# Kernel optimization log

Hardware: AMD Instinct MI355X
Metric: run time of the kernel (lower is better)

## Reference

```python
import jax, jax.numpy as jnp
import numpy as np
import math

V, D, H, F, L, S, B = 50257, 1024, 16, 4096, 4, 2048, 2
DK = D // H

def setup_inputs() -> dict:
    key = jax.random.key(0)
    ks = iter(jax.random.split(key, 32))
    std = 0.02
    def nrm(shape):
        return (std * jax.random.normal(next(ks), shape)).astype(jnp.float32)
    inp = {
        "x": jax.random.randint(next(ks), (B, S), 0, V, dtype=jnp.int32),
        "emb": nrm((V, D)),
        "ln1_g": jnp.ones((L, D), jnp.float32), "ln1_b": jnp.zeros((L, D), jnp.float32),
        "wq": nrm((L, D, D)), "wk": nrm((L, D, D)), "wv": nrm((L, D, D)), "wo": nrm((L, D, D)),
        "ln2_g": jnp.ones((L, D), jnp.float32), "ln2_b": jnp.zeros((L, D), jnp.float32),
        "w1": nrm((L, D, F)), "b1": jnp.zeros((L, F), jnp.float32),
        "w2": nrm((L, F, D)), "b2": jnp.zeros((L, D), jnp.float32),
        "lnf_g": jnp.ones((D,), jnp.float32), "lnf_b": jnp.zeros((D,), jnp.float32),
        "head_w": nrm((D, V)), "head_b": jnp.zeros((V,), jnp.float32),
    }
    return inp

def _layernorm(x, g, b, eps=1e-5):
    mu = jnp.mean(x, axis=-1, keepdims=True)
    var = jnp.var(x, axis=-1, keepdims=True)
    return (x - mu) * jax.lax.rsqrt(var + eps) * g + b

def _posenc(seq_len, d_model, dtype):
    pos = jnp.arange(seq_len, dtype=jnp.float32)[:, None]                  # [S,1]
    div = jnp.exp(jnp.arange(0, d_model, 2, dtype=jnp.float32) * (-math.log(10000.0) / d_model))
    ang = pos * div                                                        # [S,D/2]
    pe = jnp.stack([jnp.sin(ang), jnp.cos(ang)], axis=-1).reshape(seq_len, d_model)
    return pe.astype(dtype)

def reference(x, emb, ln1_g, ln1_b, wq, wk, wv, wo, ln2_g, ln2_b, w1, b1, w2, b2, lnf_g, lnf_b, head_w, head_b):
    b, s = x.shape
    h = emb[x] + _posenc(s, D, emb.dtype)[None]                            # [B,S,D]
    causal = jnp.tril(jnp.ones((s, s), dtype=bool))                       # True = keep
    scale = 1.0 / math.sqrt(DK)
    neg_inf = jnp.finfo(h.dtype).min
    for l in range(L):
        # --- attention sublayer ---
        hn = _layernorm(h, ln1_g[l], ln1_b[l])
        q = (hn @ wq[l]).reshape(b, s, H, DK)
        k = (hn @ wk[l]).reshape(b, s, H, DK)
        v = (hn @ wv[l]).reshape(b, s, H, DK)
        scores = jnp.einsum("bqhd,bkhd->bhqk", q, k) * scale
        scores = jnp.where(causal[None, None], scores, neg_inf)
        w = jax.nn.softmax(scores, axis=-1)
        attn = jnp.einsum("bhqk,bkhd->bqhd", w, v).reshape(b, s, D)
        h = h + attn @ wo[l]
        # --- FFN sublayer ---
        hn = _layernorm(h, ln2_g[l], ln2_b[l])
        h = h + jax.nn.relu(hn @ w1[l] + b1[l]) @ w2[l] + b2[l]
    h = _layernorm(h, lnf_g, lnf_b)
    logits = h @ head_w + head_b                                           # [B,S,V]
    return logits
```

## Files before the change

### kernel.cpp

```cpp
#include <hip/hip_runtime.h>
#include <math.h>

#define VOCAB 50257
#define VPAD  50432
#define DM    1024
#define NH    16
#define DKH   64
#define FF    4096
#define NL    4
#define SEQ   2048
#define BATCH 2
#define MROWS (BATCH*SEQ)

typedef __bf16 bf16_t;
typedef __bf16 bf16x8 __attribute__((ext_vector_type(8)));
typedef __bf16 bf16x4 __attribute__((ext_vector_type(4)));
typedef float  f32x4  __attribute__((ext_vector_type(4)));

typedef void as1_void __attribute__((address_space(1)));
typedef void as3_void __attribute__((address_space(3)));

__device__ __forceinline__ void gload_lds16(const void* g, void* l) {
  __builtin_amdgcn_global_load_lds((as1_void*)g, (as3_void*)l, 16, 0, 0);
}

__device__ __forceinline__ uint32_t lds_addr32(const void* p) {
  return (uint32_t)(uintptr_t)(as3_void*)p;
}

__device__ __forceinline__ bf16x8 dsr128(uint32_t addr) {
  bf16x8 v;
  asm volatile("ds_read_b128 %0, %1" : "=v"(v) : "v"(addr));
  return v;
}

#define FENCE asm volatile("" ::: "memory")
#define BAR() do { FENCE; __builtin_amdgcn_s_barrier(); FENCE; } while (0)
#define LGKM0_FENCE() do { \
  asm volatile("s_waitcnt lgkmcnt(0)" ::: "memory"); \
  __builtin_amdgcn_sched_barrier(0); \
} while (0)

__global__ __launch_bounds__(256) void embed_kernel(const int* __restrict__ x,
    const float* __restrict__ emb, float* __restrict__ h) {
  int row = blockIdx.x;
  int s = row & (SEQ - 1);
  int d = threadIdx.x * 4;
  const float* e = emb + (size_t)x[row] * DM + d;
  float4 v = *(const float4*)e;
  float vin[4] = {v.x, v.y, v.z, v.w};
  float out[4];
#pragma unroll
  for (int j = 0; j < 4; ++j) {
    int dd = d + j;
    int i = dd >> 1;
    float freq = expf(-0.017988946039016376f * (float)i);
    float ang = (float)s * freq;
    float pe = (dd & 1) ? cosf(ang) : sinf(ang);
    out[j] = vin[j] + pe;
  }
  *(float4*)(h + (size_t)row * DM + d) = make_float4(out[0], out[1], out[2], out[3]);
}

__global__ __launch_bounds__(256) void ln_kernel(const float* __restrict__ x,
    const float* __restrict__ g, const float* __restrict__ b, bf16_t* __restrict__ out) {
  int row = blockIdx.x;
  int tid = threadIdx.x, lane = tid & 63, wave = tid >> 6;
  const float* xr = x + (size_t)row * DM;
  float4 v = ((const float4*)xr)[tid];
  float s1 = v.x + v.y + v.z + v.w;
  float s2 = v.x * v.x + v.y * v.y + v.z * v.z + v.w * v.w;
#pragma unroll
  for (int d = 1; d < 64; d <<= 1) { s1 += __shfl_xor(s1, d); s2 += __shfl_xor(s2, d); }
  __shared__ float red[8];
  if (lane == 0) { red[wave] = s1; red[4 + wave] = s2; }
  __syncthreads();
  s1 = red[0] + red[1] + red[2] + red[3];
  s2 = red[4] + red[5] + red[6] + red[7];
  float mu = s1 * (1.0f / DM);
  float var = s2 * (1.0f / DM) - mu * mu;
  float rs = rsqrtf(var + 1e-5f);
  float4 gv = ((const float4*)g)[tid];
  float4 bv = ((const float4*)b)[tid];
  bf16x4 o;
  o[0] = (bf16_t)((v.x - mu) * rs * gv.x + bv.x);
  o[1] = (bf16_t)((v.y - mu) * rs * gv.y + bv.y);
  o[2] = (bf16_t)((v.z - mu) * rs * gv.z + bv.z);
  o[3] = (bf16_t)((v.w - mu) * rs * gv.w + bv.w);
  *(bf16x4*)(out + (size_t)row * DM + tid * 4) = o;
}

__global__ __launch_bounds__(256) void transpose_cast_kernel(const float* __restrict__ in,
    bf16_t* __restrict__ out, int K, int N, int Npad) {
  __shared__ float tile[32][33];
  int n0 = blockIdx.x * 32, k0 = blockIdx.y * 32;
  int tx = threadIdx.x & 31, ty = threadIdx.x >> 5;
#pragma unroll
  for (int kk = ty; kk < 32; kk += 8) {
    int n = n0 + tx;
    tile[kk][tx] = (n < N) ? in[(size_t)(k0 + kk) * N + n] : 0.f;
  }
  __syncthreads();
#pragma unroll
  for (int nn = ty; nn < 32; nn += 8) {
    out[(size_t)(n0 + nn) * K + k0 + tx] = (bf16_t)tile[tx][nn];
  }
}

__global__ __launch_bounds__(256) void vtrans_kernel(const bf16_t* __restrict__ qkv,
    bf16_t* __restrict__ vT) {
  int sb = blockIdx.x, hh = blockIdx.y, bb = blockIdx.z;
  __shared__ bf16_t t[64][72];
  int tid = threadIdx.x;
  const bf16_t* src = qkv + ((size_t)bb * SEQ + sb * 64) * (3 * DM) + 2 * DM + hh * DKH;
#pragma unroll
  for (int c = 0; c < 2; ++c) {
    int u = c * 256 + tid;
    int s = u >> 3, d8 = u & 7;
    *(bf16x8*)&t[s][d8 * 8] = *(const bf16x8*)(src + (size_t)s * (3 * DM) + d8 * 8);
  }
  __syncthreads();
  bf16_t* dst = vT + ((size_t)(bb * NH + hh) * DKH) * SEQ + sb * 64;
#pragma unroll
  for (int c = 0; c < 2; ++c) {
    int u = c * 256 + tid;
    int dk = u >> 3, s8 = u & 7;
    bf16x8 v;
#pragma unroll
    for (int j = 0; j < 8; ++j) v[j] = t[s8 * 8 + j][dk];
    *(bf16x8*)(dst + (size_t)dk * SEQ + s8 * 8) = v;
  }
}

__global__ __launch_bounds__(256) void gemm_kernel(
    const bf16_t* __restrict__ A, const bf16_t* __restrict__ Bt, int K,
    const float* __restrict__ bias, const float* __restrict__ Rsd,
    float* Cf, bf16_t* Cb, int ldc, int Nvalid, int relu) {
  __shared__ __align__(16) bf16_t lA[4096];
  __shared__ __align__(16) bf16_t lB[4096];
  int tid = threadIdx.x, lane = tid & 63, wave = tid >> 6;
  int g = lane >> 4, r = lane & 15;
  int wr = wave >> 1, wc = wave & 1;
  int m0 = blockIdx.x * 128, n0 = blockIdx.y * 128;

  f32x4 zero = {0.f, 0.f, 0.f, 0.f};
  f32x4 acc[4][4];
#pragma unroll
  for (int i = 0; i < 4; ++i)
#pragma unroll
    for (int j = 0; j < 4; ++j) acc[i][j] = zero;

  const bf16_t* Abase = A + (size_t)m0 * K;
  const bf16_t* Bbase = Bt + (size_t)n0 * K;

  for (int k0 = 0; k0 < K; k0 += 32) {
    __syncthreads();
#pragma unroll
    for (int c = 0; c < 2; ++c) {
      int u = c * 256 + tid;
      int k8 = u >> 7, rw = u & 127;
      gload_lds16(Abase + (size_t)rw * K + k0 + k8 * 8, &lA[(c * 256 + wave * 64) * 8]);
      gload_lds16(Bbase + (size_t)rw * K + k0 + k8 * 8, &lB[(c * 256 + wave * 64) * 8]);
    }
    __syncthreads();
    bf16x8 af[4], bfr[4];
#pragma unroll
    for (int mr = 0; mr < 4; ++mr)
      af[mr] = *(const bf16x8*)&lA[(g * 128 + wr * 64 + mr * 16 + r) * 8];
#pragma unroll
    for (int nr = 0; nr < 4; ++nr)
      bfr[nr] = *(const bf16x8*)&lB[(g * 128 + wc * 64 + nr * 16 + r) * 8];
#pragma unroll
    for (int mr = 0; mr < 4; ++mr)
#pragma unroll
      for (int nr = 0; nr < 4; ++nr)
        acc[mr][nr] = __builtin_amdgcn_mfma_f32_16x16x32_bf16(af[mr], bfr[nr], acc[mr][nr], 0, 0, 0);
  }

#pragma unroll
  for (int mr = 0; mr < 4; ++mr) {
    int row = m0 + wr * 64 + mr * 16 + g * 4;
#pragma unroll
    for (int nr = 0; nr < 4; ++nr) {
      int col = n0 + wc * 64 + nr * 16 + r;
      if (col < Nvalid) {
        float bval = bias ? bias[col] : 0.f;
#pragma unroll
        for (int i = 0; i < 4; ++i) {
          float vv = acc[mr][nr][i] + bval;
          if (relu) vv = fmaxf(vv, 0.f);
          size_t idx = (size_t)(row + i) * ldc + col;
          if (Rsd) vv += Rsd[idx];
          if (Cf) Cf[idx] = vv;
          if (Cb) Cb[idx] = (bf16_t)vv;
        }
      }
    }
  }
}

__global__ __launch_bounds__(512, 2) void gemm256_kernel(
    const bf16_t* __restrict__ A, const bf16_t* __restrict__ Bt, int K,
    const float* __restrict__ bias, float* Cf, bf16_t* Cb,
    int ldc, int Nvalid, int relu, int gridM, int gridN) {
  __shared__ __align__(16) bf16_t lds[65536];

  int nwg = gridM * gridN;
  int orig = blockIdx.x;
  int q = nwg >> 3, rr = nwg & 7;
  int xcd = orig & 7, idx = orig >> 3;
  int swz = (xcd < rr ? xcd * (q + 1) : rr * (q + 1) + (xcd - rr) * q) + idx;
  int bm = swz % gridM, bn = swz / gridM;
  int m0 = bm * 256, n0 = bn * 256;

  int tid = threadIdx.x, lane = tid & 63, wave = tid >> 6;
  int g = lane >> 4, r = lane & 15;
  int wr = wave >> 2, wc = wave & 3;

  f32x4 zero = {0.f, 0.f, 0.f, 0.f};
  f32x4 acc[8][4];
#pragma unroll
  for (int i = 0; i < 8; ++i)
#pragma unroll
    for (int j = 0; j < 4; ++j) acc[i][j] = zero;

  const bf16_t* Ab = A + (size_t)m0 * K;
  const bf16_t* Bb = Bt + (size_t)n0 * K;
  int NT = K >> 6;

  uint32_t L0 = lds_addr32(lds);
  uint32_t laneOff = (uint32_t)(g * 2048 + r * 16);
  uint32_t aBase0 = L0 + ((uint32_t)wr << 14) + laneOff;
  uint32_t bBase0 = L0 + 65536u + ((uint32_t)(wc >> 1) << 14) + laneOff
                  + (uint32_t)((wc & 1) * 1024);

  auto stageA = [&](int t, int hh) {
    int b = t & 1, k0 = t << 6;
    const bf16_t* src = Ab + (size_t)(hh * 128) * K + k0;
    bf16_t* dst = lds + (size_t)(b * 2 + hh) * 8192;
#pragma unroll
    for (int j = 0; j < 2; ++j) {
      int u = j * 512 + tid;
      gload_lds16(src + (size_t)(u & 127) * K + (u >> 7) * 8, dst + (j * 512 + wave * 64) * 8);
    }
  };
  auto stageB = [&](int t, int hh) {
    int b = t & 1, k0 = t << 6;
    const bf16_t* src = Bb + (size_t)(hh * 128) * K + k0;
    bf16_t* dst = lds + 32768 + (size_t)(b * 2 + hh) * 8192;
#pragma unroll
    for (int j = 0; j < 2; ++j) {
      int u = j * 512 + tid;
      gload_lds16(src + (size_t)(u & 127) * K + (u >> 7) * 8, dst + (j * 512 + wave * 64) * 8);
    }
  };

  stageB(0, 0); stageB(0, 1); stageA(0, 0); stageA(0, 1);
  if (NT > 1) {
    stageB(1, 0); stageB(1, 1);
    asm volatile("s_waitcnt vmcnt(4)" ::: "memory");
  } else {
    asm volatile("s_waitcnt vmcnt(0)" ::: "memory");
  }
  BAR();

  for (int t = 0; t < NT; ++t) {
    uint32_t bsel = (uint32_t)((t & 1) << 15);
    uint32_t Aaddr = aBase0 + bsel;
    uint32_t Baddr = bBase0 + bsel;

    bf16x8 a0[4][2], a1[4][2], b01[2][2], b23[2][2];

#pragma unroll
    for (int mi = 0; mi < 4; ++mi)
#pragma unroll
      for (int kk = 0; kk < 2; ++kk)
        a0[mi][kk] = dsr128(Aaddr + (uint32_t)(kk * 8192 + mi * 256));
#pragma unroll
    for (int ni = 0; ni < 2; ++ni)
#pragma unroll
      for (int kk = 0; kk < 2; ++kk)
        b01[ni][kk] = dsr128(Baddr + (uint32_t)(kk * 8192 + ni * 256));
    if (t + 1 < NT) stageA(t + 1, 0);
    BAR();
    LGKM0_FENCE();
    __builtin_amdgcn_s_setprio(1);
#pragma unroll
    for (int mi = 0; mi < 4; ++mi)
#pragma unroll
      for (int ni = 0; ni < 2; ++ni)
#pragma unroll
        for (int kk = 0; kk < 2; ++kk)
          acc[mi][ni] = __builtin_amdgcn_mfma_f32_16x16x32_bf16(a0[mi][kk], b01[ni][kk], acc[mi][ni], 0, 0, 0);
    __builtin_amdgcn_s_setprio(0);
    __builtin_amdgcn_sched_barrier(0);
    BAR();

#pragma unroll
    for (int ni = 0; ni < 2; ++ni)
#pragma unroll
      for (int kk = 0; kk < 2; ++kk)
        b23[ni][kk] = dsr128(Baddr + (uint32_t)(kk * 8192 + (ni + 2) * 256));
    if (t + 1 < NT) stageA(t + 1, 1);
    BAR();
    LGKM0_FENCE();
    __builtin_amdgcn_s_setprio(1);
#pragma unroll
    for (int mi = 0; mi < 4; ++mi)
#pragma unroll
      for (int ni = 0; ni < 2; ++ni)
#pragma unroll
        for (int kk = 0; kk < 2; ++kk)
          acc[mi][ni + 2] = __builtin_amdgcn_mfma_f32_16x16x32_bf16(a0[mi][kk], b23[ni][kk], acc[mi][ni + 2], 0, 0, 0);
    __builtin_amdgcn_s_setprio(0);
    __builtin_amdgcn_sched_barrier(0);
    BAR();

#pragma unroll
    for (int mi = 0; mi < 4; ++mi)
#pragma unroll
      for (int kk = 0; kk < 2; ++kk)
        a1[mi][kk] = dsr128(Aaddr + (uint32_t)(kk * 8192 + (mi + 4) * 256));
    if (t + 2 < NT) stageB(t + 2, 0);
    BAR();
    LGKM0_FENCE();
    __builtin_amdgcn_s_setprio(1);
#pragma unroll
    for (int mi = 0; mi < 4; ++mi)
#pragma unroll
      for (int ni = 0; ni < 2; ++ni)
#pragma unroll
        for (int kk = 0; kk < 2; ++kk)
          acc[mi + 4][ni] = __builtin_amdgcn_mfma_f32_16x16x32_bf16(a1[mi][kk], b01[ni][kk], acc[mi + 4][ni], 0, 0, 0);
    __builtin_amdgcn_s_setprio(0);
    __builtin_amdgcn_sched_barrier(0);
    BAR();

    if (t + 2 < NT) stageB(t + 2, 1);
    __builtin_amdgcn_sched_barrier(0);
    __builtin_amdgcn_s_setprio(1);
#pragma unroll
    for (int mi = 0; mi < 4; ++mi)
#pragma unroll
      for (int ni = 0; ni < 2; ++ni)
#pragma unroll
        for (int kk = 0; kk < 2; ++kk)
          acc[mi + 4][ni + 2] = __builtin_amdgcn_mfma_f32_16x16x32_bf16(a1[mi][kk], b23[ni][kk], acc[mi + 4][ni + 2], 0, 0, 0);
    __builtin_amdgcn_s_setprio(0);
    __builtin_amdgcn_sched_barrier(0);
    if (t + 2 < NT) {
      asm volatile("s_waitcnt vmcnt(4)" ::: "memory");
    } else {
      asm volatile("s_waitcnt vmcnt(0)" ::: "memory");
    }
    BAR();
  }

#pragma unroll
  for (int mi = 0; mi < 8; ++mi) {
    int row = m0 + wr * 128 + mi * 16 + g * 4;
#pragma unroll
    for (int ni = 0; ni < 4; ++ni) {
      int col = n0 + wc * 64 + ni * 16 + r;
      if (col < Nvalid) {
        float bval = bias ? bias[col] : 0.f;
#pragma unroll
        for (int i = 0; i < 4; ++i) {
          float vv = acc[mi][ni][i] + bval;
          if (relu) vv = fmaxf(vv, 0.f);
          size_t idxo = (size_t)(row + i) * ldc + col;
          if (Cf) Cf[idxo] = vv;
          if (Cb) Cb[idxo] = (bf16_t)vv;
        }
      }
    }
  }
}

__global__ __launch_bounds__(512, 4) void attn_kernel(const bf16_t* __restrict__ Qg,
    const bf16_t* __restrict__ Kg, const bf16_t* __restrict__ vT, bf16_t* __restrict__ Og,
    int ldq) {
  int bq = blockIdx.x, hh = blockIdx.y, bb = blockIdx.z;
  int tid = threadIdx.x, lane = tid & 63, wave = tid >> 6;
  int g = lane >> 4, r = lane & 15;
  __shared__ __align__(16) bf16_t Kl[4096];
  __shared__ __align__(16) bf16_t Vl[4096];
  __shared__ __align__(16) bf16_t Pl[8][1024];

  size_t base = (size_t)bb * SEQ * ldq + hh * DKH;
  size_t vbase = ((size_t)(bb * NH + hh)) * DKH * SEQ;
  size_t baseO = (size_t)bb * SEQ * DM + hh * DKH;
  int q0 = bq * 128 + wave * 16;
  const bf16_t* qrowp = Qg + base + (size_t)(q0 + r) * ldq;
  bf16x8 qf0 = *(const bf16x8*)(qrowp + g * 8);
  bf16x8 qf1 = *(const bf16x8*)(qrowp + 32 + g * 8);

  f32x4 zero = {0.f, 0.f, 0.f, 0.f};
  f32x4 accO[4];
#pragma unroll
  for (int dt = 0; dt < 4; ++dt) accO[dt] = zero;
  float m_i[4], l_i[4];
#pragma unroll
  for (int i = 0; i < 4; ++i) { m_i[i] = -1e30f; l_i[i] = 0.f; }
  const float scale = 0.125f;

  int skv = tid >> 3, kslot = tid & 7, kdk8 = kslot ^ (skv & 7);
  int sdk = tid >> 3, vslot = tid & 7, vkv8 = vslot ^ (sdk & 7);
  const bf16_t* ksrc0 = Kg + base + (size_t)skv * ldq + kdk8 * 8;
  const bf16_t* vsrc0 = vT + vbase + (size_t)sdk * SEQ + vkv8 * 8;

  int nkb = 2 * bq + 2;
  for (int kb = 0; kb < nkb; ++kb) {
    __syncthreads();
    gload_lds16(ksrc0 + (size_t)(kb * 64) * ldq, &Kl[(wave * 64) * 8]);
    gload_lds16(vsrc0 + kb * 64, &Vl[(wave * 64) * 8]);
    __syncthreads();

    f32x4 sc[4];
#pragma unroll
    for (int ct = 0; ct < 4; ++ct) {
      int kvrow = ct * 16 + r;
      bf16x8 kf0 = *(const bf16x8*)&Kl[(kvrow * 8 + (g ^ (r & 7))) * 8];
      bf16x8 kf1 = *(const bf16x8*)&Kl[(kvrow * 8 + ((4 + g) ^ (r & 7))) * 8];
      f32x4 s = zero;
      s = __builtin_amdgcn_mfma_f32_16x16x32_bf16(qf0, kf0, s, 0, 0, 0);
      s = __builtin_amdgcn_mfma_f32_16x16x32_bf16(qf1, kf1, s, 0, 0, 0);
      sc[ct] = s;
    }

#pragma unroll
    for (int i = 0; i < 4; ++i) {
      int qglob = q0 + g * 4 + i;
      float mx = m_i[i];
#pragma unroll
      for (int ct = 0; ct < 4; ++ct) {
        int kglob = kb * 64 + ct * 16 + r;
        float s = sc[ct][i] * scale;
        s = (kglob <= qglob) ? s : -1e30f;
        sc[ct][i] = s;
        mx = fmaxf(mx, s);
      }
#pragma unroll
      for (int d = 1; d < 16; d <<= 1) mx = fmaxf(mx, __shfl_xor(mx, d));
      float scl = __expf(m_i[i] - mx);
      l_i[i] *= scl;
      m_i[i] = mx;
      float rsum = 0.f;
#pragma unroll
      for (int ct = 0; ct < 4; ++ct) {
        float p = __expf(sc[ct][i] - mx);
        sc[ct][i] = p;
        rsum += p;
      }
#pragma unroll
      for (int d = 1; d < 16; d <<= 1) rsum += __shfl_xor(rsum, d);
      l_i[i] += rsum;
#pragma unroll
      for (int dt = 0; dt < 4; ++dt) accO[dt][i] *= scl;
    }

#pragma unroll
    for (int ct = 0; ct < 4; ++ct) {
      int kcol = ct * 16 + r;
#pragma unroll
      for (int i = 0; i < 4; ++i)
        Pl[wave][((kcol >> 3) * 16 + g * 4 + i) * 8 + (kcol & 7)] = (bf16_t)sc[ct][i];
    }

    bf16x8 pa0 = *(const bf16x8*)&Pl[wave][((0 + g) * 16 + r) * 8];
    bf16x8 pa1 = *(const bf16x8*)&Pl[wave][((4 + g) * 16 + r) * 8];
#pragma unroll
    for (int dt = 0; dt < 4; ++dt) {
      int dkrow = dt * 16 + r;
      bf16x8 vb0 = *(const bf16x8*)&Vl[(dkrow * 8 + (g ^ (r & 7))) * 8];
      bf16x8 vb1 = *(const bf16x8*)&Vl[(dkrow * 8 + ((4 + g) ^ (r & 7))) * 8];
      accO[dt] = __builtin_amdgcn_mfma_f32_16x16x32_bf16(pa0, vb0, accO[dt], 0, 0, 0);
      accO[dt] = __builtin_amdgcn_mfma_f32_16x16x32_bf16(pa1, vb1, accO[dt], 0, 0, 0);
    }
  }

#pragma unroll
  for (int dt = 0; dt < 4; ++dt)
#pragma unroll
    for (int i = 0; i < 4; ++i) {
      int rowq = q0 + g * 4 + i;
      Og[baseO + (size_t)rowq * DM + dt * 16 + r] = (bf16_t)(accO[dt][i] / l_i[i]);
    }
}

static inline void launch_gemm256(const bf16_t* A, const bf16_t* Bt, int K,
    const float* bias, float* Cf, bf16_t* Cb, int ldc, int Nvalid, int relu,
    int M, int Npad, hipStream_t stream) {
  int gridM = M / 256, gridN = Npad / 256;
  gemm256_kernel<<<dim3(gridM * gridN), 512, 0, stream>>>(
      A, Bt, K, bias, Cf, Cb, ldc, Nvalid, relu, gridM, gridN);
}

extern "C" void kernel_launch(void* const* d_in, const int* in_sizes, int n_in,
                              void* d_out, int out_size, void* d_ws, size_t ws_size,
                              hipStream_t stream) {
  const int*   x      = (const int*)d_in[0];
  const float* emb    = (const float*)d_in[1];
  const float* ln1_g  = (const float*)d_in[2];
  const float* ln1_b  = (const float*)d_in[3];
  const float* wq     = (const float*)d_in[4];
  const float* wk     = (const float*)d_in[5];
  const float* wv     = (const float*)d_in[6];
  const float* wo     = (const float*)d_in[7];
  const float* ln2_g  = (const float*)d_in[8];
  const float* ln2_b  = (const float*)d_in[9];
  const float* w1     = (const float*)d_in[10];
  const float* b1     = (const float*)d_in[11];
  const float* w2     = (const float*)d_in[12];
  const float* b2     = (const float*)d_in[13];
  const float* lnf_g  = (const float*)d_in[14];
  const float* lnf_b  = (const float*)d_in[15];
  const float* head_w = (const float*)d_in[16];
  const float* head_b = (const float*)d_in[17];
  float* out = (float*)d_out;

  char* ws = (char*)d_ws;
  size_t off = 0;
  auto alloc = [&](size_t bytes) -> void* {
    void* p = ws + off;
    off += (bytes + 255) & ~(size_t)255;
    return p;
  };
  float*  h     = (float*)alloc((size_t)MROWS * DM * 4);
  bf16_t* hn    = (bf16_t*)alloc((size_t)MROWS * DM * 2);
  bf16_t* qkv   = (bf16_t*)alloc((size_t)MROWS * 3 * DM * 2);
  bf16_t* atb   = (bf16_t*)alloc((size_t)MROWS * DM * 2);
  bf16_t* ffn1  = (bf16_t*)alloc((size_t)MROWS * FF * 2);
  bf16_t* vTb   = (bf16_t*)alloc((size_t)BATCH * NH * DKH * SEQ * 2);
  bf16_t* headT = (bf16_t*)alloc((size_t)VPAD * DM * 2);
  bf16_t* wqkvT = headT;
  bf16_t* wT    = headT + (size_t)4 * DM * DM;

  embed_kernel<<<MROWS, 256, 0, stream>>>(x, emb, h);

  for (int l = 0; l < NL; ++l) {
    ln_kernel<<<MROWS, 256, 0, stream>>>(h, ln1_g + l * DM, ln1_b + l * DM, hn);

    transpose_cast_kernel<<<dim3(DM / 32, DM / 32), 256, 0, stream>>>(
        wq + (size_t)l * DM * DM, wqkvT, DM, DM, DM);
    transpose_cast_kernel<<<dim3(DM / 32, DM / 32), 256, 0, stream>>>(
        wk + (size_t)l * DM * DM, wqkvT + (size_t)DM * DM, DM, DM, DM);
    transpose_cast_kernel<<<dim3(DM / 32, DM / 32), 256, 0, stream>>>(
        wv + (size_t)l * DM * DM, wqkvT + (size_t)2 * DM * DM, DM, DM, DM);
    launch_gemm256(hn, wqkvT, DM, nullptr, nullptr, qkv, 3 * DM, 3 * DM, 0,
                   MROWS, 3 * DM, stream);

    vtrans_kernel<<<dim3(SEQ / 64, NH, BATCH), 256, 0, stream>>>(qkv, vTb);
    attn_kernel<<<dim3(SEQ / 128, NH, BATCH), 512, 0, stream>>>(
        qkv, qkv + DM, vTb, atb, 3 * DM);

    transpose_cast_kernel<<<dim3(DM / 32, DM / 32), 256, 0, stream>>>(
        wo + (size_t)l * DM * DM, wT, DM, DM, DM);
    gemm_kernel<<<dim3(MROWS / 128, DM / 128), 256, 0, stream>>>(
        atb, wT, DM, nullptr, h, h, nullptr, DM, DM, 0);

    ln_kernel<<<MROWS, 256, 0, stream>>>(h, ln2_g + l * DM, ln2_b + l * DM, hn);

    transpose_cast_kernel<<<dim3(FF / 32, DM / 32), 256, 0, stream>>>(
        w1 + (size_t)l * DM * FF, wT, DM, FF, FF);
    launch_gemm256(hn, wT, DM, b1 + (size_t)l * FF, nullptr, ffn1, FF, FF, 1,
                   MROWS, FF, stream);

    transpose_cast_kernel<<<dim3(DM / 32, FF / 32), 256, 0, stream>>>(
        w2 + (size_t)l * FF * DM, wT, FF, DM, DM);
    gemm_kernel<<<dim3(MROWS / 128, DM / 128), 256, 0, stream>>>(
        ffn1, wT, FF, b2 + (size_t)l * DM, h, h, nullptr, DM, DM, 0);
  }

  ln_kernel<<<MROWS, 256, 0, stream>>>(h, lnf_g, lnf_b, hn);
  transpose_cast_kernel<<<dim3(VPAD / 32, DM / 32), 256, 0, stream>>>(
      head_w, headT, DM, VOCAB, VPAD);
  launch_gemm256(hn, headT, DM, head_b, out, nullptr, VOCAB, VOCAB, 0,
                 MROWS, VPAD, stream);
}
```

Baseline: 2.644 ms.

## Double-buffer the 128x128 GEMM, swizzle tiles per XCD, merge QKV transposes

The 128-tile GEMM used for the Wo and W2 projections is rewritten to double-buffer its LDS tiles. Global-to-LDS loads for step t+2 are issued while MFMAs run on step t, and blocks are remapped with an XCD-aware swizzle for better L2 locality. The three separate Q/K/V weight transpose launches are merged into one launch with a z-grid, and attention query blocks are dispatched in reverse order so the longest causal blocks start first. Costs are twice the LDS per block and hand-managed waitcnt and barrier logic that must stay correct.

```diff
diff --git a/kernel.cpp b/kernel.cpp
--- a/kernel.cpp
+++ b/kernel.cpp
@@ -107,6 +107,23 @@
   }
 }
 
+__global__ __launch_bounds__(256) void qkvtrans_kernel(const float* __restrict__ wq,
+    const float* __restrict__ wk, const float* __restrict__ wv, bf16_t* __restrict__ out) {
+  __shared__ float tile[32][33];
+  int z = blockIdx.z;
+  const float* in = (z == 0) ? wq : (z == 1) ? wk : wv;
+  bf16_t* dst = out + (size_t)z * DM * DM;
+  int n0 = blockIdx.x * 32, k0 = blockIdx.y * 32;
+  int tx = threadIdx.x & 31, ty = threadIdx.x >> 5;
+#pragma unroll
+  for (int kk = ty; kk < 32; kk += 8)
+    tile[kk][tx] = in[(size_t)(k0 + kk) * DM + n0 + tx];
+  __syncthreads();
+#pragma unroll
+  for (int nn = ty; nn < 32; nn += 8)
+    dst[(size_t)(n0 + nn) * DM + k0 + tx] = (bf16_t)tile[tx][nn];
+}
+
 __global__ __launch_bounds__(256) void vtrans_kernel(const bf16_t* __restrict__ qkv,
     bf16_t* __restrict__ vT) {
   int sb = blockIdx.x, hh = blockIdx.y, bb = blockIdx.z;
@@ -132,16 +149,23 @@
   }
 }
 
-__global__ __launch_bounds__(256) void gemm_kernel(
+__global__ __launch_bounds__(256) void gemm128_kernel(
     const bf16_t* __restrict__ A, const bf16_t* __restrict__ Bt, int K,
     const float* __restrict__ bias, const float* __restrict__ Rsd,
-    float* Cf, bf16_t* Cb, int ldc, int Nvalid, int relu) {
-  __shared__ __align__(16) bf16_t lA[4096];
-  __shared__ __align__(16) bf16_t lB[4096];
+    float* Cf, bf16_t* Cb, int ldc, int Nvalid, int relu, int gridM, int gridN) {
+  __shared__ __align__(16) bf16_t lds[16384];
+
+  int nwg = gridM * gridN;
+  int orig = blockIdx.x;
+  int q = nwg >> 3, rr = nwg & 7;
+  int xcd = orig & 7, idx = orig >> 3;
+  int swz = (xcd < rr ? xcd * (q + 1) : rr * (q + 1) + (xcd - rr) * q) + idx;
+  int bm = swz % gridM, bn = swz / gridM;
+  int m0 = bm * 128, n0 = bn * 128;
+
   int tid = threadIdx.x, lane = tid & 63, wave = tid >> 6;
   int g = lane >> 4, r = lane & 15;
   int wr = wave >> 1, wc = wave & 1;
-  int m0 = blockIdx.x * 128, n0 = blockIdx.y * 128;
 
   f32x4 zero = {0.f, 0.f, 0.f, 0.f};
   f32x4 acc[4][4];
@@ -152,29 +176,60 @@
 
   const bf16_t* Abase = A + (size_t)m0 * K;
   const bf16_t* Bbase = Bt + (size_t)n0 * K;
-
-  for (int k0 = 0; k0 < K; k0 += 32) {
-    __syncthreads();
-#pragma unroll
-    for (int c = 0; c < 2; ++c) {
-      int u = c * 256 + tid;
-      int k8 = u >> 7, rw = u & 127;
-      gload_lds16(Abase + (size_t)rw * K + k0 + k8 * 8, &lA[(c * 256 + wave * 64) * 8]);
-      gload_lds16(Bbase + (size_t)rw * K + k0 + k8 * 8, &lB[(c * 256 + wave * 64) * 8]);
-    }
-    __syncthreads();
+  int NT = K >> 5;
+
+  uint32_t L0 = lds_addr32(lds);
+  uint32_t aF = L0 + (uint32_t)((g * 128 + wr * 64 + r) * 16);
+  uint32_t bF = L0 + 16384u + (uint32_t)((g * 128 + wc * 64 + r) * 16);
+
+  auto stage = [&](int t) {
+    int b = t & 1, k0 = t << 5;
+    bf16_t* dA = lds + (size_t)b * 4096;
+    bf16_t* dB = lds + 8192 + (size_t)b * 4096;
+#pragma unroll
+    for (int j = 0; j < 2; ++j) {
+      int u = j * 256 + tid;
+      int row = u & 127, k8 = u >> 7;
+      gload_lds16(Abase + (size_t)row * K + k0 + k8 * 8, dA + (j * 256 + wave * 64) * 8);
+    }
+#pragma unroll
+    for (int j = 0; j < 2; ++j) {
+      int u = j * 256 + tid;
+      int row = u & 127, k8 = u >> 7;
+      gload_lds16(Bbase + (size_t)row * K + k0 + k8 * 8, dB + (j * 256 + wave * 64) * 8);
+    }
+  };
+
+  stage(0);
+  if (NT > 1) stage(1);
+  asm volatile("s_waitcnt vmcnt(4)" ::: "memory");
+  if (NT == 1) { asm volatile("s_waitcnt vmcnt(0)" ::: "memory"); }
+  BAR();
+
+  for (int t = 0; t < NT; ++t) {
+    uint32_t boff = (uint32_t)((t & 1) << 13);
     bf16x8 af[4], bfr[4];
 #pragma unroll
-    for (int mr = 0; mr < 4; ++mr)
-      af[mr] = *(const bf16x8*)&lA[(g * 128 + wr * 64 + mr * 16 + r) * 8];
-#pragma unroll
-    for (int nr = 0; nr < 4; ++nr)
-      bfr[nr] = *(const bf16x8*)&lB[(g * 128 + wc * 64 + nr * 16 + r) * 8];
+    for (int mr = 0; mr < 4; ++mr) af[mr] = dsr128(aF + boff + (uint32_t)(mr * 256));
+#pragma unroll
+    for (int nr = 0; nr < 4; ++nr) bfr[nr] = dsr128(bF + boff + (uint32_t)(nr * 256));
+    LGKM0_FENCE();
+    BAR();
+    if (t + 2 < NT) stage(t + 2);
+    __builtin_amdgcn_s_setprio(1);
 #pragma unroll
     for (int mr = 0; mr < 4; ++mr)
 #pragma unroll
       for (int nr = 0; nr < 4; ++nr)
         acc[mr][nr] = __builtin_amdgcn_mfma_f32_16x16x32_bf16(af[mr], bfr[nr], acc[mr][nr], 0, 0, 0);
+    __builtin_amdgcn_s_setprio(0);
+    __builtin_amdgcn_sched_barrier(0);
+    if (t + 2 < NT) {
+      asm volatile("s_waitcnt vmcnt(4)" ::: "memory");
+    } else {
+      asm volatile("s_waitcnt vmcnt(0)" ::: "memory");
+    }
+    BAR();
   }
 
 #pragma unroll
@@ -189,10 +244,10 @@
         for (int i = 0; i < 4; ++i) {
           float vv = acc[mr][nr][i] + bval;
           if (relu) vv = fmaxf(vv, 0.f);
-          size_t idx = (size_t)(row + i) * ldc + col;
-          if (Rsd) vv += Rsd[idx];
-          if (Cf) Cf[idx] = vv;
-          if (Cb) Cb[idx] = (bf16_t)vv;
+          size_t idxo = (size_t)(row + i) * ldc + col;
+          if (Rsd) vv += Rsd[idxo];
+          if (Cf) Cf[idxo] = vv;
+          if (Cb) Cb[idxo] = (bf16_t)vv;
         }
       }
     }
@@ -380,7 +435,8 @@
 __global__ __launch_bounds__(512, 4) void attn_kernel(const bf16_t* __restrict__ Qg,
     const bf16_t* __restrict__ Kg, const bf16_t* __restrict__ vT, bf16_t* __restrict__ Og,
     int ldq) {
-  int bq = blockIdx.x, hh = blockIdx.y, bb = blockIdx.z;
+  int bq = (int)gridDim.x - 1 - (int)blockIdx.x;
+  int hh = blockIdx.y, bb = blockIdx.z;
   int tid = threadIdx.x, lane = tid & 63, wave = tid >> 6;
   int g = lane >> 4, r = lane & 15;
   __shared__ __align__(16) bf16_t Kl[4096];
@@ -494,6 +550,14 @@
   int gridM = M / 256, gridN = Npad / 256;
   gemm256_kernel<<<dim3(gridM * gridN), 512, 0, stream>>>(
       A, Bt, K, bias, Cf, Cb, ldc, Nvalid, relu, gridM, gridN);
+}
+
+static inline void launch_gemm128(const bf16_t* A, const bf16_t* Bt, int K,
+    const float* bias, const float* Rsd, float* Cf, bf16_t* Cb,
+    int ldc, int Nvalid, int relu, int M, int Npad, hipStream_t stream) {
+  int gridM = M / 128, gridN = Npad / 128;
+  gemm128_kernel<<<dim3(gridM * gridN), 256, 0, stream>>>(
+      A, Bt, K, bias, Rsd, Cf, Cb, ldc, Nvalid, relu, gridM, gridN);
 }
 
 extern "C" void kernel_launch(void* const* d_in, const int* in_sizes, int n_in,
@@ -541,12 +605,8 @@
   for (int l = 0; l < NL; ++l) {
     ln_kernel<<<MROWS, 256, 0, stream>>>(h, ln1_g + l * DM, ln1_b + l * DM, hn);
 
-    transpose_cast_kernel<<<dim3(DM / 32, DM / 32), 256, 0, stream>>>(
-        wq + (size_t)l * DM * DM, wqkvT, DM, DM, DM);
-    transpose_cast_kernel<<<dim3(DM / 32, DM / 32), 256, 0, stream>>>(
-        wk + (size_t)l * DM * DM, wqkvT + (size_t)DM * DM, DM, DM, DM);
-    transpose_cast_kernel<<<dim3(DM / 32, DM / 32), 256, 0, stream>>>(
-        wv + (size_t)l * DM * DM, wqkvT + (size_t)2 * DM * DM, DM, DM, DM);
+    qkvtrans_kernel<<<dim3(DM / 32, DM / 32, 3), 256, 0, stream>>>(
+        wq + (size_t)l * DM * DM, wk + (size_t)l * DM * DM, wv + (size_t)l * DM * DM, wqkvT);
     launch_gemm256(hn, wqkvT, DM, nullptr, nullptr, qkv, 3 * DM, 3 * DM, 0,
                    MROWS, 3 * DM, stream);
 
@@ -556,8 +616,7 @@
 
     transpose_cast_kernel<<<dim3(DM / 32, DM / 32), 256, 0, stream>>>(
         wo + (size_t)l * DM * DM, wT, DM, DM, DM);
-    gemm_kernel<<<dim3(MROWS / 128, DM / 128), 256, 0, stream>>>(
-        atb, wT, DM, nullptr, h, h, nullptr, DM, DM, 0);
+    launch_gemm128(atb, wT, DM, nullptr, h, h, nullptr, DM, DM, 0, MROWS, DM, stream);
 
     ln_kernel<<<MROWS, 256, 0, stream>>>(h, ln2_g + l * DM, ln2_b + l * DM, hn);
 
@@ -568,8 +627,8 @@
 
     transpose_cast_kernel<<<dim3(DM / 32, FF / 32), 256, 0, stream>>>(
         w2 + (size_t)l * FF * DM, wT, FF, DM, DM);
-    gemm_kernel<<<dim3(MROWS / 128, DM / 128), 256, 0, stream>>>(
-        ffn1, wT, FF, b2 + (size_t)l * DM, h, h, nullptr, DM, DM, 0);
+    launch_gemm128(ffn1, wT, FF, b2 + (size_t)l * DM, h, h, nullptr, DM, DM, 0,
+                   MROWS, DM, stream);
   }
 
   ln_kernel<<<MROWS, 256, 0, stream>>>(h, lnf_g, lnf_b, hn);
```

Measured after the change: 2.331 ms. 1.13x faster.
